# Optimization experiments

Measured on AMD Instinct MI355X. Metric: run time of the kernel, lower is better.

The kernel has to match this reference:

```python
import jax, jax.numpy as jnp
import numpy as np

N_NODES = 10   # 1 input (I:0) + 8 hidden (H:0..H:7) + 1 output (O:0), topological order
D = 64         # per-node feature dim (all nodes share dim 64)
B = 65536      # batch size


def setup_inputs() -> dict:
    key = jax.random.key(0)
    k1, k2, k3 = jax.random.split(key, 3)
    x = jax.random.normal(k1, (B, D), dtype=jnp.float32)
    # Dense packing of per-edge Linear weights: edge (f -> t) uses W[f, t] (shape [D, D])
    # and bias b[f, t] (shape [D]); only f < t entries are ever read (upper-tri DAG).
    W = jax.random.normal(k2, (N_NODES, N_NODES, D, D), dtype=jnp.float32) * (1.0 / np.sqrt(D))
    b = jax.random.normal(k3, (N_NODES, N_NODES, D), dtype=jnp.float32) * 0.02
    return {"x": x, "W": W, "b": b}


def reference(x, W, b):
    # WiredLayer.forward with a full upper-triangular connection DAG:
    # node t's activation = sum over all earlier nodes f of Linear_{f->t}(act_f).
    acts = [x]  # inputs['I:0'] = x  (single input node)
    for t in range(1, N_NODES):  # fixed small structural loop over nodes
        preds = jnp.stack(acts)                    # [t, B, D] activations of all predecessors
        x_t = jnp.einsum('fbd,fdh->bh', preds, W[:t, t]) + b[:t, t].sum(axis=0)
        acts.append(x_t)
    return acts[-1]  # single output node 'O:0'
```

## Files before the change

### kernel.cpp

```cpp
#include <hip/hip_runtime.h>

#define D 64
#define NN 10

typedef __bf16 bf16x8 __attribute__((ext_vector_type(8)));
typedef float f32x4 __attribute__((ext_vector_type(4)));

__global__ __launch_bounds__(256) void wired_build(const float* __restrict__ W,
                                                   const float* __restrict__ Bv,
                                                   float* __restrict__ Mc) {
  __shared__ __align__(16) float hist[NN][D];
  __shared__ float part[4][D];
  const int r = blockIdx.x;
  const int lane = threadIdx.x & 63;
  const int w = threadIdx.x >> 6;

  if (threadIdx.x < D)
    hist[0][threadIdx.x] = (r < D && threadIdx.x == r) ? 1.0f : 0.0f;
  __syncthreads();

  for (int t = 1; t < NN; ++t) {
    float a0 = 0.f, a1 = 0.f, a2 = 0.f, a3 = 0.f;
    for (int f = w; f < t; f += 4) {
      const float* wft = W + (size_t)(f * NN + t) * D * D;
      const float4* h4 = (const float4*)hist[f];
#pragma unroll
      for (int k4 = 0; k4 < 16; ++k4) {
        float4 h = h4[k4];
        a0 += h.x * wft[(k4 * 4 + 0) * D + lane];
        a1 += h.y * wft[(k4 * 4 + 1) * D + lane];
        a2 += h.z * wft[(k4 * 4 + 2) * D + lane];
        a3 += h.w * wft[(k4 * 4 + 3) * D + lane];
      }
      if (r == D) a0 += Bv[(f * NN + t) * D + lane];
    }
    part[w][lane] = (a0 + a1) + (a2 + a3);
    __syncthreads();
    if (w == 0)
      hist[t][lane] = part[0][lane] + part[1][lane] + part[2][lane] + part[3][lane];
    __syncthreads();
  }

  if (threadIdx.x < D)
    Mc[r * D + threadIdx.x] = hist[NN - 1][threadIdx.x];
}

__global__ __launch_bounds__(256) void wired_apply(const float* __restrict__ x,
                                                   const float* __restrict__ Mc,
                                                   float* __restrict__ out,
                                                   int nrows) {
  const int lane = threadIdx.x & 63;
  const int wave = threadIdx.x >> 6;
  const int l15 = lane & 15;
  const int quad = lane >> 4;

  bf16x8 bfrag[2][4];
#pragma unroll
  for (int kc = 0; kc < 2; ++kc) {
#pragma unroll
    for (int nc = 0; nc < 4; ++nc) {
      bf16x8 bb;
#pragma unroll
      for (int j = 0; j < 8; ++j) {
        bb[j] = (__bf16)Mc[(kc * 32 + quad * 8 + j) * D + nc * 16 + l15];
      }
      bfrag[kc][nc] = bb;
    }
  }
  float cfrag[4];
#pragma unroll
  for (int nc = 0; nc < 4; ++nc) cfrag[nc] = Mc[D * D + nc * 16 + l15];

  const int gw = blockIdx.x * 4 + wave;
  const int nw = gridDim.x * 4;
  const int ntiles = nrows >> 4;
  for (int tile = gw; tile < ntiles; tile += nw) {
    const float* xr = x + (size_t)(tile * 16 + l15) * D + quad * 8;
    float4 v0 = *(const float4*)(xr);
    float4 v1 = *(const float4*)(xr + 4);
    float4 v2 = *(const float4*)(xr + 32);
    float4 v3 = *(const float4*)(xr + 36);
    bf16x8 af0, af1;
    af0[0] = (__bf16)v0.x; af0[1] = (__bf16)v0.y; af0[2] = (__bf16)v0.z; af0[3] = (__bf16)v0.w;
    af0[4] = (__bf16)v1.x; af0[5] = (__bf16)v1.y; af0[6] = (__bf16)v1.z; af0[7] = (__bf16)v1.w;
    af1[0] = (__bf16)v2.x; af1[1] = (__bf16)v2.y; af1[2] = (__bf16)v2.z; af1[3] = (__bf16)v2.w;
    af1[4] = (__bf16)v3.x; af1[5] = (__bf16)v3.y; af1[6] = (__bf16)v3.z; af1[7] = (__bf16)v3.w;

#pragma unroll
    for (int nc = 0; nc < 4; ++nc) {
      f32x4 acc = {0.f, 0.f, 0.f, 0.f};
      acc = __builtin_amdgcn_mfma_f32_16x16x32_bf16(af0, bfrag[0][nc], acc, 0, 0, 0);
      acc = __builtin_amdgcn_mfma_f32_16x16x32_bf16(af1, bfrag[1][nc], acc, 0, 0, 0);
#pragma unroll
      for (int rr = 0; rr < 4; ++rr) {
        out[(size_t)(tile * 16 + quad * 4 + rr) * D + nc * 16 + l15] =
            acc[rr] + cfrag[nc];
      }
    }
  }
}

extern "C" void kernel_launch(void* const* d_in, const int* in_sizes, int n_in,
                              void* d_out, int out_size, void* d_ws, size_t ws_size,
                              hipStream_t stream) {
  const float* x = (const float*)d_in[0];
  const float* W = (const float*)d_in[1];
  const float* Bv = (const float*)d_in[2];
  float* out = (float*)d_out;
  float* Mc = (float*)d_ws;
  const int nrows = in_sizes[0] / D;

  wired_build<<<65, 256, 0, stream>>>(W, Bv, Mc);
  wired_apply<<<256, 256, 0, stream>>>(x, Mc, out, nrows);
}
```

Before: 89.56 us.

## Pre-pack bf16 MFMA fragments in build and transpose apply for vector stores

The build kernel now writes the collapsed matrix already packed as bf16 MFMA fragments, plus a separate bias vector, so the apply kernel loads each fragment with one 16-byte load instead of converting scalars. Build splits the K dimension across waves rather than predecessors, double-buffers the partial sums to drop one barrier, and fully unrolls the node loop. Apply swaps the MFMA operand roles so each lane holds four consecutive output columns and writes float4 stores, seeds the accumulator with the bias, and launches one 16-row tile per wave instead of a grid-stride loop. The trade-offs are many more blocks and a per-block fragment reload.

```diff
diff --git a/kernel.cpp b/kernel.cpp
--- a/kernel.cpp
+++ b/kernel.cpp
@@ -6,97 +6,98 @@
 typedef __bf16 bf16x8 __attribute__((ext_vector_type(8)));
 typedef float f32x4 __attribute__((ext_vector_type(4)));
 
+
 __global__ __launch_bounds__(256) void wired_build(const float* __restrict__ W,
                                                    const float* __restrict__ Bv,
-                                                   float* __restrict__ Mc) {
-  __shared__ __align__(16) float hist[NN][D];
-  __shared__ float part[4][D];
+                                                   __bf16* __restrict__ Apack,
+                                                   float* __restrict__ cvec) {
+  __shared__ float hist[NN][D];
+  __shared__ float part[2][4][D];
   const int r = blockIdx.x;
   const int lane = threadIdx.x & 63;
   const int w = threadIdx.x >> 6;
 
-  if (threadIdx.x < D)
-    hist[0][threadIdx.x] = (r < D && threadIdx.x == r) ? 1.0f : 0.0f;
+  hist[0][lane] = (r < D && lane == r) ? 1.0f : 0.0f;
   __syncthreads();
 
+#pragma unroll
   for (int t = 1; t < NN; ++t) {
     float a0 = 0.f, a1 = 0.f, a2 = 0.f, a3 = 0.f;
-    for (int f = w; f < t; f += 4) {
-      const float* wft = W + (size_t)(f * NN + t) * D * D;
-      const float4* h4 = (const float4*)hist[f];
 #pragma unroll
-      for (int k4 = 0; k4 < 16; ++k4) {
-        float4 h = h4[k4];
-        a0 += h.x * wft[(k4 * 4 + 0) * D + lane];
-        a1 += h.y * wft[(k4 * 4 + 1) * D + lane];
-        a2 += h.z * wft[(k4 * 4 + 2) * D + lane];
-        a3 += h.w * wft[(k4 * 4 + 3) * D + lane];
+    for (int f = 0; f < t; ++f) {
+      const float* wft = W + (size_t)(f * NN + t) * D * D + w * 16 * D + lane;
+      const float* hf = &hist[f][w * 16];
+#pragma unroll
+      for (int kk = 0; kk < 16; kk += 4) {
+        a0 += hf[kk + 0] * wft[(kk + 0) * D];
+        a1 += hf[kk + 1] * wft[(kk + 1) * D];
+        a2 += hf[kk + 2] * wft[(kk + 2) * D];
+        a3 += hf[kk + 3] * wft[(kk + 3) * D];
       }
-      if (r == D) a0 += Bv[(f * NN + t) * D + lane];
+      if (r == D && w == 0) a0 += Bv[(f * NN + t) * D + lane];
     }
-    part[w][lane] = (a0 + a1) + (a2 + a3);
+    part[t & 1][w][lane] = (a0 + a1) + (a2 + a3);
     __syncthreads();
-    if (w == 0)
-      hist[t][lane] = part[0][lane] + part[1][lane] + part[2][lane] + part[3][lane];
-    __syncthreads();
+    float s = part[t & 1][0][lane] + part[t & 1][1][lane] +
+              part[t & 1][2][lane] + part[t & 1][3][lane];
+    hist[t][lane] = s;
   }
 
-  if (threadIdx.x < D)
-    Mc[r * D + threadIdx.x] = hist[NN - 1][threadIdx.x];
+  if (threadIdx.x < D) {
+    float v = hist[NN - 1][threadIdx.x];
+    if (r < D) {
+      const int kc = r >> 5, q = (r >> 3) & 3, j = r & 7;
+      const int nc = threadIdx.x >> 4, l15 = threadIdx.x & 15;
+      Apack[(size_t)(((kc * 4 + nc) * 64) + q * 16 + l15) * 8 + j] = (__bf16)v;
+    } else {
+      cvec[threadIdx.x] = v;
+    }
+  }
 }
 
 __global__ __launch_bounds__(256) void wired_apply(const float* __restrict__ x,
-                                                   const float* __restrict__ Mc,
+                                                   const __bf16* __restrict__ Apack,
+                                                   const float* __restrict__ cvec,
                                                    float* __restrict__ out,
-                                                   int nrows) {
+                                                   int ntiles) {
   const int lane = threadIdx.x & 63;
   const int wave = threadIdx.x >> 6;
   const int l15 = lane & 15;
   const int quad = lane >> 4;
 
-  bf16x8 bfrag[2][4];
+  bf16x8 afrag[2][4];
 #pragma unroll
-  for (int kc = 0; kc < 2; ++kc) {
+  for (int kc = 0; kc < 2; ++kc)
 #pragma unroll
-    for (int nc = 0; nc < 4; ++nc) {
-      bf16x8 bb;
+    for (int nc = 0; nc < 4; ++nc)
+      afrag[kc][nc] = *(const bf16x8*)(Apack + (size_t)(((kc * 4 + nc) * 64) + lane) * 8);
+
+  float4 cq[4];
 #pragma unroll
-      for (int j = 0; j < 8; ++j) {
-        bb[j] = (__bf16)Mc[(kc * 32 + quad * 8 + j) * D + nc * 16 + l15];
-      }
-      bfrag[kc][nc] = bb;
-    }
-  }
-  float cfrag[4];
+  for (int nc = 0; nc < 4; ++nc)
+    cq[nc] = *(const float4*)(cvec + nc * 16 + quad * 4);
+
+  const int tile = blockIdx.x * 4 + wave;
+  if (tile >= ntiles) return;
+
+  const float* xr = x + (size_t)(tile * 16 + l15) * D + quad * 8;
+  float4 v0 = *(const float4*)(xr);
+  float4 v1 = *(const float4*)(xr + 4);
+  float4 v2 = *(const float4*)(xr + 32);
+  float4 v3 = *(const float4*)(xr + 36);
+  bf16x8 bf0, bf1;
+  bf0[0] = (__bf16)v0.x; bf0[1] = (__bf16)v0.y; bf0[2] = (__bf16)v0.z; bf0[3] = (__bf16)v0.w;
+  bf0[4] = (__bf16)v1.x; bf0[5] = (__bf16)v1.y; bf0[6] = (__bf16)v1.z; bf0[7] = (__bf16)v1.w;
+  bf1[0] = (__bf16)v2.x; bf1[1] = (__bf16)v2.y; bf1[2] = (__bf16)v2.z; bf1[3] = (__bf16)v2.w;
+  bf1[4] = (__bf16)v3.x; bf1[5] = (__bf16)v3.y; bf1[6] = (__bf16)v3.z; bf1[7] = (__bf16)v3.w;
+
+  float* orow = out + (size_t)(tile * 16 + l15) * D + quad * 4;
 #pragma unroll
-  for (int nc = 0; nc < 4; ++nc) cfrag[nc] = Mc[D * D + nc * 16 + l15];
-
-  const int gw = blockIdx.x * 4 + wave;
-  const int nw = gridDim.x * 4;
-  const int ntiles = nrows >> 4;
-  for (int tile = gw; tile < ntiles; tile += nw) {
-    const float* xr = x + (size_t)(tile * 16 + l15) * D + quad * 8;
-    float4 v0 = *(const float4*)(xr);
-    float4 v1 = *(const float4*)(xr + 4);
-    float4 v2 = *(const float4*)(xr + 32);
-    float4 v3 = *(const float4*)(xr + 36);
-    bf16x8 af0, af1;
-    af0[0] = (__bf16)v0.x; af0[1] = (__bf16)v0.y; af0[2] = (__bf16)v0.z; af0[3] = (__bf16)v0.w;
-    af0[4] = (__bf16)v1.x; af0[5] = (__bf16)v1.y; af0[6] = (__bf16)v1.z; af0[7] = (__bf16)v1.w;
-    af1[0] = (__bf16)v2.x; af1[1] = (__bf16)v2.y; af1[2] = (__bf16)v2.z; af1[3] = (__bf16)v2.w;
-    af1[4] = (__bf16)v3.x; af1[5] = (__bf16)v3.y; af1[6] = (__bf16)v3.z; af1[7] = (__bf16)v3.w;
-
-#pragma unroll
-    for (int nc = 0; nc < 4; ++nc) {
-      f32x4 acc = {0.f, 0.f, 0.f, 0.f};
-      acc = __builtin_amdgcn_mfma_f32_16x16x32_bf16(af0, bfrag[0][nc], acc, 0, 0, 0);
-      acc = __builtin_amdgcn_mfma_f32_16x16x32_bf16(af1, bfrag[1][nc], acc, 0, 0, 0);
-#pragma unroll
-      for (int rr = 0; rr < 4; ++rr) {
-        out[(size_t)(tile * 16 + quad * 4 + rr) * D + nc * 16 + l15] =
-            acc[rr] + cfrag[nc];
-      }
-    }
+  for (int nc = 0; nc < 4; ++nc) {
+    f32x4 acc = {cq[nc].x, cq[nc].y, cq[nc].z, cq[nc].w};
+    acc = __builtin_amdgcn_mfma_f32_16x16x32_bf16(afrag[0][nc], bf0, acc, 0, 0, 0);
+    acc = __builtin_amdgcn_mfma_f32_16x16x32_bf16(afrag[1][nc], bf1, acc, 0, 0, 0);
+    *(float4*)(orow + nc * 16) = {acc[0], acc[1], acc[2], acc[3]};
   }
 }
 
@@ -107,9 +108,14 @@
   const float* W = (const float*)d_in[1];
   const float* Bv = (const float*)d_in[2];
   float* out = (float*)d_out;
-  float* Mc = (float*)d_ws;
+
+  __bf16* Apack = (__bf16*)d_ws;
+  float* cvec = (float*)((char*)d_ws + 8192);
+
   const int nrows = in_sizes[0] / D;
+  const int ntiles = nrows / 16;
+  const int nblocks = (ntiles + 3) / 4;
 
-  wired_build<<<65, 256, 0, stream>>>(W, Bv, Mc);
-  wired_apply<<<256, 256, 0, stream>>>(x, Mc, out, nrows);
+  wired_build<<<65, 256, 0, stream>>>(W, Bv, Apack, cvec);
+  wired_apply<<<nblocks, 256, 0, stream>>>(x, Apack, cvec, out, ntiles);
 }
```

After: 94.62 us. 5.7% more time.
